# Kernel optimization log

Hardware: AMD Instinct MI355X
Metric: run time of the kernel (lower is better)

Reference implementation:

```python
import jax, jax.numpy as jnp
import numpy as np

N_TOKEN = 267735
HEAD = 20000
CUTOFFS = [20000, 20008, 20016, 200000, 267735]  # from cl_root_leaf_dict with 2 roots of 8 leaves
N_ROOTS = 2


def setup_inputs() -> dict:
    key = jax.random.key(0)
    k1, k2, k3, k4 = jax.random.split(key, 4)
    N, D = 1024, 1024
    hidden = jax.random.normal(k1, (N, D), dtype=jnp.float32)
    target = jax.random.randint(k2, (N,), 0, N_TOKEN)
    W = jax.random.normal(k3, (N_TOKEN, D), dtype=jnp.float32) * 0.02
    b = jnp.zeros((N_TOKEN,), dtype=jnp.float32)
    cluster_weight = jax.random.normal(k4, (2, D), dtype=jnp.float32) * 0.02
    cluster_bias = jnp.zeros((2,), dtype=jnp.float32)
    return {"hidden": hidden, "target": target, "W": W, "b": b,
            "cluster_weight": cluster_weight, "cluster_bias": cluster_bias}


def _nll(hidden, target, W, b, cw, cb):
    cutoff_ends = [0] + CUTOFFS
    # head = first 20000 vocab rows + 2 cluster rows (d_proj == d_embed -> no projection)
    head_w = jnp.concatenate([W[:HEAD], cw], axis=0)          # [20002, D]
    head_b = jnp.concatenate([b[:HEAD], cb], axis=0)          # [20002]
    head_lp = jax.nn.log_softmax(hidden @ head_w.T + head_b, axis=-1)  # [N, 20002]
    n_head_cols = head_lp.shape[1]
    rows = jnp.arange(hidden.shape[0])
    # segment 0: target in [0, 20000) -> nll directly from head log-probs
    lp0 = head_lp[rows, jnp.clip(target, 0, HEAD - 1)]
    nll = -lp0  # only valid where target < HEAD; overwritten below otherwise
    for i in range(1, len(CUTOFFS)):
        l, r = cutoff_ends[i], cutoff_ends[i + 1]
        # per-segment tail logits for all tokens (masked combine keeps shapes static)
        tail_lp = jax.nn.log_softmax(hidden @ W[l:r].T + b[l:r], axis=-1)  # [N, r-l]
        # routing column exactly as in the torch code:
        # j = i-1 for root segments, -(i - n_roots) for the two cluster segments
        j = (i - 1) if i <= N_ROOTS else (n_head_cols - (i - N_ROOTS))
        lp_i = head_lp[:, j] + tail_lp[rows, jnp.clip(target - l, 0, r - l - 1)]
        mask = (target >= l) & (target < r)
        nll = jnp.where(mask, -lp_i, nll)
    return nll


def reference(hidden, target, W, b, cluster_weight, cluster_bias):
    return _nll(hidden, target, W, b, cluster_weight, cluster_bias)
```

## Files before the change

kernel.cpp:

```cpp
#include <hip/hip_runtime.h>
#include <hip/hip_bf16.h>

#define D_DIM 1024
#define NTOK 267735
#define NEXT_ 267737
#define HEADN 20000

typedef __attribute__((ext_vector_type(8))) short bf16x8;
typedef __attribute__((ext_vector_type(4))) float f32x4;
typedef __attribute__((ext_vector_type(4))) unsigned uint4v;

__device__ __forceinline__ int seg_of(int c){
  if (c < HEADN)  return 0;
  if (c < 20008)  return 1;
  if (c < 20016)  return 2;
  if (c < 200000) return 3;
  if (c < NTOK)   return 4;
  return 0;
}

__device__ __forceinline__ unsigned pack2(float x, float y){
  __hip_bfloat16 a = __float2bfloat16(x);
  __hip_bfloat16 b = __float2bfloat16(y);
  unsigned short ua = *reinterpret_cast<unsigned short*>(&a);
  unsigned short ub = *reinterpret_cast<unsigned short*>(&b);
  return (unsigned)ua | ((unsigned)ub << 16);
}

#define BM 256
#define BN 128
#define BK 32
#define NTHREADS 512
#define KSTEPS (D_DIM/BK)
#define NCOLT 2092
#define NBLK 8384

#define APRIME_OFF 32768
#define APRIME_BYTES (1024*1024*2)

__device__ __forceinline__ void stage16(const float* g, unsigned short* l){
  __builtin_amdgcn_global_load_lds(
      (const __attribute__((address_space(1))) void*)g,
      (__attribute__((address_space(3))) void*)l, 16, 0, 0);
}

__global__ void prep_convert(const float* __restrict__ hidden,
                             unsigned short* __restrict__ Ap)
{
  int t = blockIdx.x * blockDim.x + threadIdx.x;
  int r16 = t & 15, kc = (t >> 4) & 127, rb = t >> 11;
  const float4* src = reinterpret_cast<const float4*>(hidden + ((size_t)(rb*16 + r16) * D_DIM + kc*8));
  float4 x = src[0], y = src[1];
  uint4 o;
  o.x = pack2(x.x, x.y); o.y = pack2(x.z, x.w);
  o.z = pack2(y.x, y.y); o.w = pack2(y.z, y.w);
  reinterpret_cast<uint4*>(Ap)[t] = o;
}

__global__ __launch_bounds__(NTHREADS, 1) void gemm_lse_adir(
    const unsigned short* __restrict__ Ap, const float* __restrict__ W,
    const float* __restrict__ bias,   const float* __restrict__ cw,
    const float* __restrict__ cb,     float* __restrict__ accg)
{
  const int b = blockIdx.x;
  const int k8 = b & 7;
  const int sq_ = b >> 3;
  const int xb = sq_ & 3;
  const int yb = (sq_ >> 2) * 8 + k8;
  if (yb >= NCOLT) return;

  __shared__ unsigned short lsB0[BN * 64];
  __shared__ unsigned short lsB1[BN * 64];

  const int tid = threadIdx.x;
  const int rowBase = xb * BM;
  const int colBase = yb * BN;

  const int lane = tid & 63;
  const int wv = tid >> 6;
  const int wm = wv >> 1;
  const int wn = wv & 1;
  const int q  = lane >> 4;
  const int r16 = lane & 15;

  const float* sp0; const float* sp1;
  {
    int f = tid;        int row = f >> 3; int kc = (f & 7) ^ (row & 7);
    int c = colBase + row;
    const float* base = (c < NTOK)  ? (W  + (size_t)c * D_DIM)
                      : (c < NEXT_) ? (cw + (size_t)(c - NTOK) * D_DIM) : W;
    sp0 = base + kc*4;
  }
  {
    int f = 512 + tid;  int row = f >> 3; int kc = (f & 7) ^ (row & 7);
    int c = colBase + row;
    const float* base = (c < NTOK)  ? (W  + (size_t)c * D_DIM)
                      : (c < NEXT_) ? (cw + (size_t)(c - NTOK) * D_DIM) : W;
    sp1 = base + kc*4;
  }
  const int dst0 = wv*512;
  const int dst1 = 4096 + wv*512;

#define STAGE(Lbuf, kn) do{ \
    stage16(sp0 + (kn)*BK, &Lbuf[dst0]); \
    stage16(sp1 + (kn)*BK, &Lbuf[dst1]); }while(0)

  int loO[4], hiO[4];
#pragma unroll
  for (int j=0;j<4;++j){
    int row = wn*64 + j*16 + r16;
    loO[j] = row*64 + (((2*q  ) ^ (row & 7)) << 3);
    hiO[j] = row*64 + (((2*q+1) ^ (row & 7)) << 3);
  }

  const unsigned short* a0 = Ap + (size_t)(xb*16 + wm*4 + 0)*16384 + q*128 + r16*8;
  const unsigned short* a1 = Ap + (size_t)(xb*16 + wm*4 + 1)*16384 + q*128 + r16*8;
  const unsigned short* a2 = Ap + (size_t)(xb*16 + wm*4 + 2)*16384 + q*128 + r16*8;
  const unsigned short* a3 = Ap + (size_t)(xb*16 + wm*4 + 3)*16384 + q*128 + r16*8;

  f32x4 acc[4][4];
#pragma unroll
  for (int i=0;i<4;++i)
#pragma unroll
    for (int j=0;j<4;++j) acc[i][j] = (f32x4){0.f,0.f,0.f,0.f};

#define BFRAG(Lr, j, out) { \
    float4 lo = *reinterpret_cast<const float4*>(&Lr[loO[j]]); \
    float4 hi = *reinterpret_cast<const float4*>(&Lr[hiO[j]]); \
    uint4v uu; \
    uu.x = pack2(lo.x, lo.y); uu.y = pack2(lo.z, lo.w); \
    uu.z = pack2(hi.x, hi.y); uu.w = pack2(hi.z, hi.w); \
    out = __builtin_bit_cast(bf16x8, uu); }

  STAGE(lsB0, 0);
  __syncthreads();

  for (int kt = 0; kt < KSTEPS; ++kt){
    unsigned short* Lr = (kt & 1) ? lsB1 : lsB0;
    unsigned short* Lw = (kt & 1) ? lsB0 : lsB1;

    bf16x8 af0 = *reinterpret_cast<const bf16x8*>(a0 + kt*512);
    bf16x8 af1 = *reinterpret_cast<const bf16x8*>(a1 + kt*512);
    bf16x8 af2 = *reinterpret_cast<const bf16x8*>(a2 + kt*512);
    bf16x8 af3 = *reinterpret_cast<const bf16x8*>(a3 + kt*512);

    if (kt + 1 < KSTEPS) STAGE(Lw, kt+1);

    bf16x8 b0, b1, b2, b3;
    BFRAG(Lr, 0, b0); BFRAG(Lr, 1, b1); BFRAG(Lr, 2, b2); BFRAG(Lr, 3, b3);

    acc[0][0] = __builtin_amdgcn_mfma_f32_16x16x32_bf16(af0, b0, acc[0][0], 0,0,0);
    acc[0][1] = __builtin_amdgcn_mfma_f32_16x16x32_bf16(af0, b1, acc[0][1], 0,0,0);
    acc[0][2] = __builtin_amdgcn_mfma_f32_16x16x32_bf16(af0, b2, acc[0][2], 0,0,0);
    acc[0][3] = __builtin_amdgcn_mfma_f32_16x16x32_bf16(af0, b3, acc[0][3], 0,0,0);
    acc[1][0] = __builtin_amdgcn_mfma_f32_16x16x32_bf16(af1, b0, acc[1][0], 0,0,0);
    acc[1][1] = __builtin_amdgcn_mfma_f32_16x16x32_bf16(af1, b1, acc[1][1], 0,0,0);
    acc[1][2] = __builtin_amdgcn_mfma_f32_16x16x32_bf16(af1, b2, acc[1][2], 0,0,0);
    acc[1][3] = __builtin_amdgcn_mfma_f32_16x16x32_bf16(af1, b3, acc[1][3], 0,0,0);
    acc[2][0] = __builtin_amdgcn_mfma_f32_16x16x32_bf16(af2, b0, acc[2][0], 0,0,0);
    acc[2][1] = __builtin_amdgcn_mfma_f32_16x16x32_bf16(af2, b1, acc[2][1], 0,0,0);
    acc[2][2] = __builtin_amdgcn_mfma_f32_16x16x32_bf16(af2, b2, acc[2][2], 0,0,0);
    acc[2][3] = __builtin_amdgcn_mfma_f32_16x16x32_bf16(af2, b3, acc[2][3], 0,0,0);
    acc[3][0] = __builtin_amdgcn_mfma_f32_16x16x32_bf16(af3, b0, acc[3][0], 0,0,0);
    acc[3][1] = __builtin_amdgcn_mfma_f32_16x16x32_bf16(af3, b1, acc[3][1], 0,0,0);
    acc[3][2] = __builtin_amdgcn_mfma_f32_16x16x32_bf16(af3, b2, acc[3][2], 0,0,0);
    acc[3][3] = __builtin_amdgcn_mfma_f32_16x16x32_bf16(af3, b3, acc[3][3], 0,0,0);

    __syncthreads();
  }

  int sq[4]; float bq[4];
#pragma unroll
  for (int f=0; f<4; ++f){
    int c = colBase + wn*64 + f*16 + r16;
    if (c < NTOK)       { sq[f] = seg_of(c); bq[f] = bias[c]; }
    else if (c < NEXT_) { sq[f] = 0;         bq[f] = cb[c - NTOK]; }
    else                { sq[f] = -1;        bq[f] = 0.f; }
  }
  int sfirst = seg_of(colBase);
  int clast  = colBase + BN - 1; if (clast > NEXT_-1) clast = NEXT_-1;
  int slast  = seg_of(clast);
  int smin = sfirst, smax = slast;
  if (slast < sfirst){ smin = 0; smax = 4; }

#pragma unroll
  for (int i=0;i<4;++i){
#pragma unroll
    for (int r=0;r<4;++r){
      float e[4];
#pragma unroll
      for (int f=0;f<4;++f) e[f] = __expf(acc[i][f][r] + bq[f]);
      int rowg = rowBase + wm*64 + i*16 + (lane>>4)*4 + r;
      for (int s2 = smin; s2 <= smax; ++s2){
        float p = 0.f;
#pragma unroll
        for (int f=0;f<4;++f) p += (sq[f]==s2) ? e[f] : 0.f;
#pragma unroll
        for (int off=1; off<16; off<<=1) p += __shfl_xor(p, off, 16);
        if ((lane & 15) == 0 && p != 0.f) atomicAdd(&accg[rowg*8 + s2], p);
      }
    }
  }
}

__global__ __launch_bounds__(256) void finalize_kernel(
    const float* __restrict__ hidden, const int* __restrict__ target,
    const float* __restrict__ W,      const float* __restrict__ bias,
    const float* __restrict__ cw,     const float* __restrict__ cb,
    const float* __restrict__ accg,   float* __restrict__ out)
{
  const int row  = blockIdx.x * 4 + (threadIdx.x >> 6);
  const int lane = threadIdx.x & 63;
  const int t = target[row];

  const float4* h4 = reinterpret_cast<const float4*>(hidden + (size_t)row * D_DIM);
  const float4* w1 = reinterpret_cast<const float4*>(W + (size_t)t * D_DIM);
  int s = 0; const float* jraw = W; float jb = 0.f;
  if (t >= HEADN){
    if      (t < 20008)  { s=1; jraw = W;          jb = bias[0]; }
    else if (t < 20016)  { s=2; jraw = W + D_DIM;  jb = bias[1]; }
    else if (t < 200000) { s=3; jraw = cw + D_DIM; jb = cb[1];   }
    else                 { s=4; jraw = cw;         jb = cb[0];   }
  }
  const float4* w2 = reinterpret_cast<const float4*>(jraw);

  float p1 = 0.f, p2 = 0.f;
#pragma unroll
  for (int j=0;j<4;++j){
    float4 hv = h4[lane + 64*j];
    float4 av = w1[lane + 64*j];
    float4 bv = w2[lane + 64*j];
    p1 += hv.x*av.x + hv.y*av.y + hv.z*av.z + hv.w*av.w;
    p2 += hv.x*bv.x + hv.y*bv.y + hv.z*bv.z + hv.w*bv.w;
  }
#pragma unroll
  for (int off=32; off; off>>=1){
    p1 += __shfl_xor(p1, off, 64);
    p2 += __shfl_xor(p2, off, 64);
  }

  if (lane == 0){
    float lseH = __logf(accg[row*8 + 0]);
    float nll;
    if (t < HEADN){
      nll = -(p1 + bias[t] - lseH);
    } else {
      float lseS = __logf(accg[row*8 + s]);
      nll = -((p2 + jb - lseH) + (p1 + bias[t] - lseS));
    }
    out[row] = nll;
  }
}

extern "C" void kernel_launch(void* const* d_in, const int* in_sizes, int n_in,
                              void* d_out, int out_size, void* d_ws, size_t ws_size,
                              hipStream_t stream)
{
  const float* hidden = (const float*)d_in[0];
  const int*   target = (const int*)  d_in[1];
  const float* W      = (const float*)d_in[2];
  const float* bias   = (const float*)d_in[3];
  const float* cw     = (const float*)d_in[4];
  const float* cb     = (const float*)d_in[5];
  float* out  = (float*)d_out;
  float* accg = (float*)d_ws;
  unsigned short* Ap = (unsigned short*)((char*)d_ws + APRIME_OFF);

  hipMemsetAsync(accg, 0, 1024*8*sizeof(float), stream);

  prep_convert<<<512, 256, 0, stream>>>(hidden, Ap);
  gemm_lse_adir<<<NBLK, NTHREADS, 0, stream>>>(Ap, W, bias, cw, cb, accg);
  finalize_kernel<<<256, 256, 0, stream>>>(hidden, target, W, bias, cw, cb, accg, out);
}
```

Measured before the change: 887.5 us.

## Restage W tiles as two k-halves with new swizzle and hardware bf16 pack

Changes how each thread stages W rows into shared memory: one row pointer per thread loads the two 16-float k-halves into separate LDS halves, with a new XOR swizzle and matching fragment read offsets. It also replaces the software float-to-bf16 packing with the v_cvt_pk_bf16_f32 instruction. The aim is to cut address computation, improve global coalescing and LDS bank behaviour, and shorten the conversion instruction sequence. The risk is a wrong swizzle or offset mapping, and rounding that differs from the old pack2 path.

```diff
diff --git a/kernel.cpp b/kernel.cpp
--- a/kernel.cpp
+++ b/kernel.cpp
@@ -43,6 +43,8 @@
       (const __attribute__((address_space(1))) void*)g,
       (__attribute__((address_space(3))) void*)l, 16, 0, 0);
 }
+
+#define CVTPK(d, x, y) asm("v_cvt_pk_bf16_f32 %0, %1, %2" : "=v"(d) : "v"(x), "v"(y))
 
 __global__ void prep_convert(const float* __restrict__ hidden,
                              unsigned short* __restrict__ Ap)
@@ -83,34 +85,30 @@
   const int q  = lane >> 4;
   const int r16 = lane & 15;
 
-  const float* sp0; const float* sp1;
+  const float* sp;
   {
-    int f = tid;        int row = f >> 3; int kc = (f & 7) ^ (row & 7);
-    int c = colBase + row;
-    const float* base = (c < NTOK)  ? (W  + (size_t)c * D_DIM)
-                      : (c < NEXT_) ? (cw + (size_t)(c - NTOK) * D_DIM) : W;
-    sp0 = base + kc*4;
-  }
-  {
-    int f = 512 + tid;  int row = f >> 3; int kc = (f & 7) ^ (row & 7);
-    int c = colBase + row;
-    const float* base = (c < NTOK)  ? (W  + (size_t)c * D_DIM)
-                      : (c < NEXT_) ? (cw + (size_t)(c - NTOK) * D_DIM) : W;
-    sp1 = base + kc*4;
-  }
-  const int dst0 = wv*512;
-  const int dst1 = 4096 + wv*512;
+    int srow = wv*16 + (lane >> 2);
+    int c    = (lane & 3) ^ ((srow >> 1) & 3);
+    int col  = colBase + srow;
+    const float* base = (col < NTOK)  ? (W  + (size_t)col * D_DIM)
+                      : (col < NEXT_) ? (cw + (size_t)(col - NTOK) * D_DIM) : W;
+    sp = base + c*4;
+  }
+  const int dstH0 = wv*512;
+  const int dstH1 = 4096 + wv*512;
 
 #define STAGE(Lbuf, kn) do{ \
-    stage16(sp0 + (kn)*BK, &Lbuf[dst0]); \
-    stage16(sp1 + (kn)*BK, &Lbuf[dst1]); }while(0)
+    stage16(sp + (kn)*BK,      &Lbuf[dstH0]); \
+    stage16(sp + (kn)*BK + 16, &Lbuf[dstH1]); }while(0)
 
   int loO[4], hiO[4];
 #pragma unroll
   for (int j=0;j<4;++j){
     int row = wn*64 + j*16 + r16;
-    loO[j] = row*64 + (((2*q  ) ^ (row & 7)) << 3);
-    hiO[j] = row*64 + (((2*q+1) ^ (row & 7)) << 3);
+    int swz = (row >> 1) & 3;
+    int h   = q >> 1;
+    loO[j] = h*4096 + row*32 + (((2*q  ) & 3) ^ swz)*8;
+    hiO[j] = h*4096 + row*32 + (((2*q+1) & 3) ^ swz)*8;
   }
 
   const unsigned short* a0 = Ap + (size_t)(xb*16 + wm*4 + 0)*16384 + q*128 + r16*8;
@@ -127,9 +125,10 @@
 #define BFRAG(Lr, j, out) { \
     float4 lo = *reinterpret_cast<const float4*>(&Lr[loO[j]]); \
     float4 hi = *reinterpret_cast<const float4*>(&Lr[hiO[j]]); \
-    uint4v uu; \
-    uu.x = pack2(lo.x, lo.y); uu.y = pack2(lo.z, lo.w); \
-    uu.z = pack2(hi.x, hi.y); uu.w = pack2(hi.z, hi.w); \
+    unsigned u0,u1,u2,u3; \
+    CVTPK(u0, lo.x, lo.y); CVTPK(u1, lo.z, lo.w); \
+    CVTPK(u2, hi.x, hi.y); CVTPK(u3, hi.z, hi.w); \
+    uint4v uu; uu.x=u0; uu.y=u1; uu.z=u2; uu.w=u3; \
     out = __builtin_bit_cast(bf16x8, uu); }
 
   STAGE(lsB0, 0);
```

After: 830.7 us. 1.07x faster.
